# Performance work log

Hardware: AMD Instinct MI355X
Metric: run time of the kernel (lower is better)

Reference implementation:

```python
import jax, jax.numpy as jnp
import numpy as np

EPS = 1e-5

def _ln(x, g, b, axes):
    mu = x.mean(axis=axes, keepdims=True)
    var = ((x - mu) ** 2).mean(axis=axes, keepdims=True)
    return (x - mu) * jax.lax.rsqrt(var + EPS) * g + b

def _conv1d(x, w, b, groups=1):
    # x: (B, C, L), w: (O, I/groups, K), padding=1
    y = jax.lax.conv_general_dilated(x, w, (1,), [(1, 1)],
                                     dimension_numbers=('NCH', 'OIH', 'NCH'),
                                     feature_group_count=groups)
    return y + b[None, :, None]

def _gelu(x):
    return jax.nn.gelu(x, approximate=False)

def _ssm(x, xproj_w, xproj_b, A, D, sn_g, sn_b):
    # x: (B, L, d_inner)
    n = A.shape[-1]
    xp = jnp.einsum('bld,nd->bln', x, xproj_w) + xproj_b   # (B, L, 2n)
    Bp = jnp.tanh(xp[..., :n])
    Cp = jnp.tanh(xp[..., n:])
    tA = jnp.tanh(A)                                        # (d_inner, n)
    Bsz, L, di = x.shape
    state0 = jnp.zeros((Bsz, di, n), x.dtype)

    def step(state, inputs):
        Bt, Ct, xt = inputs                 # (B,n), (B,n), (B,di)
        state = state + Bt[:, None, :]      # broadcast over d_inner
        out = jnp.einsum('bdn,bn->bd', state, Ct) + xt * D
        state = state * tA[None]
        state = _ln(state, sn_g, sn_b, (1, 2))  # LayerNorm over [d_inner, d_state]
        return state, out

    xs = (jnp.swapaxes(Bp, 0, 1), jnp.swapaxes(Cp, 0, 1), jnp.swapaxes(x, 0, 1))
    _, ys = jax.lax.scan(step, state0, xs)  # ys: (L, B, di)
    return jnp.swapaxes(ys, 0, 1)

def _mamba_block(h, inproj_w, inproj_b, dw_w, dw_b, xproj_w, xproj_b, A, D, sn_g, sn_b, outproj_w, outproj_b):
    di = dw_w.shape[0]
    xp = jnp.einsum('bld,ed->ble', h, inproj_w) + inproj_b  # (B, L, 2*di)
    x_conv, x_res = xp[..., :di], xp[..., di:]
    x_conv = _gelu(_conv1d(jnp.swapaxes(x_conv, 1, 2), dw_w, dw_b, groups=di))
    x_conv = jnp.swapaxes(x_conv, 1, 2)
    y = _ssm(x_conv, xproj_w, xproj_b, A, D, sn_g, sn_b)
    y = y * _gelu(x_res)
    return jnp.einsum('bld,od->blo', y, outproj_w) + outproj_b

def setup_inputs() -> dict:
    key = jax.random.key(0)
    ks = jax.random.split(key, 10)
    B, L, Cin, dm, nl, di, n, nc = 128, 400, 8, 256, 2, 512, 16, 37
    rn = lambda k, shp, s: jax.random.normal(k, shp, jnp.float32) * s
    return {
        'x': jax.random.normal(ks[0], (B, L, Cin), jnp.float32),
        'conv1_w': rn(ks[1], (dm, Cin, 3), 0.1), 'conv1_b': jnp.zeros((dm,), jnp.float32),
        'conv2_w': rn(ks[2], (dm, dm, 3), 0.05), 'conv2_b': jnp.zeros((dm,), jnp.float32),
        'ln_g': jnp.ones((nl, dm), jnp.float32), 'ln_b': jnp.zeros((nl, dm), jnp.float32),
        'inproj_w': rn(ks[3], (nl, 2 * di, dm), 0.02), 'inproj_b': jnp.zeros((nl, 2 * di), jnp.float32),
        'dw_w': rn(ks[4], (nl, di, 1, 3), 0.1), 'dw_b': jnp.zeros((nl, di), jnp.float32),
        'xproj_w': rn(ks[5], (nl, 2 * n, di), 0.02), 'xproj_b': jnp.zeros((nl, 2 * n), jnp.float32),
        'A': jnp.full((nl, di, n), 0.1, jnp.float32), 'D': jnp.ones((nl, di), jnp.float32),
        'sn_g': jnp.ones((nl, di, n), jnp.float32), 'sn_b': jnp.zeros((nl, di, n), jnp.float32),
        'outproj_w': rn(ks[6], (nl, dm, di), 0.02), 'outproj_b': jnp.zeros((nl, dm), jnp.float32),
        'fc_w': rn(ks[7], (nc, dm), 0.02), 'fc_b': jnp.zeros((nc,), jnp.float32),
    }

def reference(x, conv1_w, conv1_b, conv2_w, conv2_b, ln_g, ln_b, inproj_w, inproj_b,
              dw_w, dw_b, xproj_w, xproj_b, A, D, sn_g, sn_b, outproj_w, outproj_b,
              fc_w, fc_b):
    h = jnp.swapaxes(x, 1, 2)                      # (B, Cin, L)
    h = jax.nn.relu(_conv1d(h, conv1_w, conv1_b))
    h = jax.nn.relu(_conv1d(h, conv2_w, conv2_b))
    h = jnp.swapaxes(h, 1, 2)                      # (B, L, d_model)
    n_layers = ln_g.shape[0]
    for i in range(n_layers):
        hn = _ln(h, ln_g[i], ln_b[i], (-1,))
        h = h + _mamba_block(hn, inproj_w[i], inproj_b[i], dw_w[i], dw_b[i],
                             xproj_w[i], xproj_b[i], A[i], D[i], sn_g[i], sn_b[i],
                             outproj_w[i], outproj_b[i])
    pooled = h.mean(axis=1)                        # (B, d_model)
    return pooled @ fc_w.T + fc_b                  # (B, num_classes)
```

## Files before the change

kernel.cpp:

```cpp
#include <hip/hip_runtime.h>
#include <hip/hip_bf16.h>
#include <math.h>

#define DEVINL __device__ __forceinline__

typedef __attribute__((ext_vector_type(2))) float  f32x2;
typedef __attribute__((ext_vector_type(4))) float  f32x4;
typedef __attribute__((ext_vector_type(8))) __bf16 bf16x8;
typedef __attribute__((ext_vector_type(8))) unsigned short ushort8;

DEVINL float b2f(unsigned short u) {
    union { unsigned int i; float f; } v; v.i = ((unsigned int)u) << 16; return v.f;
}
DEVINL unsigned short f2b(float f) {
    union { float f; unsigned int i; } v; v.f = f;
    unsigned int u = v.i;
    unsigned int r = (u + 0x7fffu + ((u >> 16) & 1u)) >> 16;
    return (unsigned short)r;
}
DEVINL float gelu_exact(float x) {
    return 0.5f * x * (1.0f + erff(x * 0.70710678118654752440f));
}

DEVINL f32x2 pk_fma(f32x2 a, f32x2 b, f32x2 c) {
    f32x2 d; asm("v_pk_fma_f32 %0, %1, %2, %3" : "=v"(d) : "v"(a), "v"(b), "v"(c)); return d;
}
DEVINL f32x2 pk_add(f32x2 a, f32x2 b) {
    f32x2 d; asm("v_pk_add_f32 %0, %1, %2" : "=v"(d) : "v"(a), "v"(b)); return d;
}
DEVINL f32x2 pk_mul(f32x2 a, f32x2 b) {
    f32x2 d; asm("v_pk_mul_f32 %0, %1, %2" : "=v"(d) : "v"(a), "v"(b)); return d;
}

DEVINL void bar_lgkm() {
    asm volatile("s_waitcnt lgkmcnt(0)" ::: "memory");
    __builtin_amdgcn_s_barrier();
    __builtin_amdgcn_sched_barrier(0);
}

DEVINL int swz(int off) { return off ^ (((off >> 6) & 7) << 3); }

DEVINL void gload16(const unsigned short* g, unsigned short* l) {
    __builtin_amdgcn_global_load_lds(
        (const __attribute__((address_space(1))) unsigned int*)g,
        (__attribute__((address_space(3))) unsigned int*)l, 16, 0, 0);
}

template <int CTRL>
DEVINL float dpp_add(float x) {
    int xi = __builtin_bit_cast(int, x);
    int yi = __builtin_amdgcn_update_dpp(0, xi, CTRL, 0xf, 0xf, true);
    return x + __builtin_bit_cast(float, yi);
}
DEVINL float wave_sum63(float x) {
    x = dpp_add<0x111>(x);
    x = dpp_add<0x112>(x);
    x = dpp_add<0x114>(x);
    x = dpp_add<0x118>(x);
    x = dpp_add<0x142>(x);
    x = dpp_add<0x143>(x);
    return x;
}

__global__ __launch_bounds__(256) void conv1_kernel(
    const float* __restrict__ x, const float* __restrict__ w,
    const float* __restrict__ bias, unsigned short* __restrict__ h1)
{
    __shared__ float xs[52 * 8];
    int b = blockIdx.x >> 3, tile = blockIdx.x & 7;
    int p0 = tile * 50;
    int t = threadIdx.x;
    for (int i = t; i < 416; i += 256) {
        int p = i >> 3, c = i & 7;
        int lp = p0 + p - 1;
        xs[i] = (lp >= 0 && lp < 400) ? x[((size_t)b * 400 + lp) * 8 + c] : 0.0f;
    }
    float wr[24];
    const float4* wp = (const float4*)(w + t * 24);
#pragma unroll
    for (int i = 0; i < 6; ++i) {
        float4 v4 = wp[i];
        wr[i * 4] = v4.x; wr[i * 4 + 1] = v4.y; wr[i * 4 + 2] = v4.z; wr[i * 4 + 3] = v4.w;
    }
    float bs = bias[t];
    __syncthreads();
#pragma unroll 2
    for (int p = 0; p < 50; ++p) {
        float acc = bs;
#pragma unroll
        for (int dt = 0; dt < 3; ++dt)
#pragma unroll
            for (int c = 0; c < 8; ++c)
                acc += xs[(p + dt) * 8 + c] * wr[c * 3 + dt];
        h1[((size_t)b * 400 + p0 + p) * 256 + t] = f2b(fmaxf(acc, 0.0f));
    }
}

__global__ void reorder_w2_kernel(const float* __restrict__ w, unsigned short* __restrict__ out)
{
    int idx = blockIdx.x * 256 + threadIdx.x;
    if (idx >= 256 * 768) return;
    int o = idx / 768, r = idx % 768;
    int tpos = r / 256, ci = r % 256;
    out[idx] = f2b(w[o * 768 + ci * 3 + tpos]);
}

__global__ void castw_kernel(const float* __restrict__ in, unsigned short* __restrict__ out, int n)
{
    int i = blockIdx.x * 256 + threadIdx.x;
    if (i < n) out[i] = f2b(in[i]);
}

__global__ __launch_bounds__(256) void ln_kernel(
    const float* __restrict__ h, const float* __restrict__ g,
    const float* __restrict__ bta, unsigned short* __restrict__ out)
{
    int w = threadIdx.x >> 6, l = threadIdx.x & 63;
    int row = blockIdx.x * 4 + w;
    const float* p = h + (size_t)row * 256 + l * 4;
    float4 v = *(const float4*)p;
    float s  = v.x + v.y + v.z + v.w;
    float s2 = v.x * v.x + v.y * v.y + v.z * v.z + v.w * v.w;
#pragma unroll
    for (int m = 1; m < 64; m <<= 1) { s += __shfl_xor(s, m); s2 += __shfl_xor(s2, m); }
    float mu = s * (1.0f / 256.0f);
    float var = s2 * (1.0f / 256.0f) - mu * mu;
    float rs = rsqrtf(var + 1e-5f);
    float4 gg = *(const float4*)(g + l * 4);
    float4 bb = *(const float4*)(bta + l * 4);
    ushort4 o;
    o.x = f2b((v.x - mu) * rs * gg.x + bb.x);
    o.y = f2b((v.y - mu) * rs * gg.y + bb.y);
    o.z = f2b((v.z - mu) * rs * gg.z + bb.z);
    o.w = f2b((v.w - mu) * rs * gg.w + bb.w);
    *(ushort4*)(out + (size_t)row * 256 + l * 4) = o;
}

template <int EPI>
__global__ __launch_bounds__(256) void gemm_bt(
    const unsigned short* __restrict__ A, const unsigned short* __restrict__ Bt,
    const float* __restrict__ bias, const float* __restrict__ res,
    void* __restrict__ Cout, int N, int K, int lda, int ldc)
{
    __shared__ unsigned short As[128 * 64];
    __shared__ unsigned short Bs[128 * 64];
    const int nbn = N >> 7;
    int bm = blockIdx.x / nbn, bn = blockIdx.x % nbn;
    int t = threadIdx.x, l = t & 63, w = t >> 6;
    int wm = w & 1, wn = w >> 1;
    int srow = t >> 3;
    int scol = 8 * ((t & 7) ^ ((t >> 3) & 7));
    f32x4 acc[4][4] = {};
    const int ktn = K >> 6;
    for (int kt = 0; kt < ktn; ++kt) {
#pragma unroll
        for (int i = 0; i < 4; ++i) {
            int row = i * 32 + srow;
            gload16(A + (size_t)(bm * 128 + row) * lda + kt * 64 + scol,
                    As + (i * 256 + w * 64) * 8);
            gload16(Bt + (size_t)(bn * 128 + row) * K + kt * 64 + scol,
                    Bs + (i * 256 + w * 64) * 8);
        }
        __syncthreads();
#pragma unroll
        for (int kk = 0; kk < 2; ++kk) {
            bf16x8 af[4], bfr[4];
#pragma unroll
            for (int i = 0; i < 4; ++i) {
                af[i]  = *(const bf16x8*)(As + swz((wm * 64 + i * 16 + (l & 15)) * 64 + kk * 32 + (l >> 4) * 8));
                bfr[i] = *(const bf16x8*)(Bs + swz((wn * 64 + i * 16 + (l & 15)) * 64 + kk * 32 + (l >> 4) * 8));
            }
#pragma unroll
            for (int i = 0; i < 4; ++i)
#pragma unroll
                for (int j = 0; j < 4; ++j)
                    acc[i][j] = __builtin_amdgcn_mfma_f32_16x16x32_bf16(af[i], bfr[j], acc[i][j], 0, 0, 0);
        }
        __syncthreads();
    }
    int r0 = bm * 128 + wm * 64 + (l >> 4) * 4;
    int c0 = bn * 128 + wn * 64 + (l & 15);
#pragma unroll
    for (int i = 0; i < 4; ++i) {
#pragma unroll
        for (int j = 0; j < 4; ++j) {
            int col = c0 + j * 16;
            float bb = bias[col];
#pragma unroll
            for (int q = 0; q < 4; ++q) {
                int row = r0 + i * 16 + q;
                float v = acc[i][j][q] + bb;
                if (EPI == 0) {
                    ((unsigned short*)Cout)[(size_t)row * ldc + col] = f2b(v);
                } else if (EPI == 1) {
                    ((unsigned short*)Cout)[(size_t)row * ldc + col] = f2b(gelu_exact(v));
                } else if (EPI == 3) {
                    size_t idx = (size_t)row * ldc + col;
                    ((float*)Cout)[idx] = v + res[idx];
                } else {
                    if (col < 512)
                        ((unsigned short*)Cout)[(size_t)row * 512 + col] = f2b(v);
                    else
                        ((unsigned short*)res)[(size_t)row * 512 + (col - 512)] = f2b(gelu_exact(v));
                }
            }
        }
    }
}

__global__ __launch_bounds__(256) void gemm_conv2(
    const unsigned short* __restrict__ h1, const unsigned short* __restrict__ Bt,
    const float* __restrict__ bias, float* __restrict__ Cout)
{
    __shared__ unsigned short As[128 * 64];
    __shared__ unsigned short Bs[128 * 64];
    int bm = blockIdx.x >> 1, bn = blockIdx.x & 1;
    int t = threadIdx.x, l = t & 63, w = t >> 6;
    int wm = w & 1, wn = w >> 1;
    f32x4 acc[4][4] = {};
    for (int kt = 0; kt < 12; ++kt) {
        int tpos = kt >> 2;
        int cbase = (kt & 3) * 64;
#pragma unroll
        for (int i = 0; i < 4; ++i) {
            int off = (i * 256 + t) * 8;
            int row = off >> 6, col = off & 63;
            int m = bm * 128 + row;
            int b = m / 400, ll = m % 400;
            int lp = ll + tpos - 1;
            ushort8 va = (ushort8)0;
            if (lp >= 0 && lp < 400)
                va = *(const ushort8*)(h1 + ((size_t)(b * 400 + lp) * 256 + cbase + col));
            *(ushort8*)(As + swz(off)) = va;
            ushort8 vb = *(const ushort8*)(Bt + (size_t)(bn * 128 + row) * 768 + kt * 64 + col);
            *(ushort8*)(Bs + swz(off)) = vb;
        }
        __syncthreads();
#pragma unroll
        for (int kk = 0; kk < 2; ++kk) {
            bf16x8 af[4], bfr[4];
#pragma unroll
            for (int i = 0; i < 4; ++i) {
                af[i]  = *(const bf16x8*)(As + swz((wm * 64 + i * 16 + (l & 15)) * 64 + kk * 32 + (l >> 4) * 8));
                bfr[i] = *(const bf16x8*)(Bs + swz((wn * 64 + i * 16 + (l & 15)) * 64 + kk * 32 + (l >> 4) * 8));
            }
#pragma unroll
            for (int i = 0; i < 4; ++i)
#pragma unroll
                for (int j = 0; j < 4; ++j)
                    acc[i][j] = __builtin_amdgcn_mfma_f32_16x16x32_bf16(af[i], bfr[j], acc[i][j], 0, 0, 0);
        }
        __syncthreads();
    }
    int r0 = bm * 128 + wm * 64 + (l >> 4) * 4;
    int c0 = bn * 128 + wn * 64 + (l & 15);
#pragma unroll
    for (int i = 0; i < 4; ++i)
#pragma unroll
        for (int j = 0; j < 4; ++j) {
            int col = c0 + j * 16;
            float bb = bias[col];
#pragma unroll
            for (int q = 0; q < 4; ++q) {
                int row = r0 + i * 16 + q;
                Cout[(size_t)row * 256 + col] = fmaxf(acc[i][j][q] + bb, 0.0f);
            }
        }
}

__global__ __launch_bounds__(256) void dwconv_kernel(
    const unsigned short* __restrict__ xp, const float* __restrict__ w,
    const float* __restrict__ bias, unsigned short* __restrict__ out)
{
    int b = blockIdx.x >> 3, tile = blockIdx.x & 7;
    int p0 = tile * 50;
    int t = threadIdx.x;
    int c = t * 2;
    float w00 = w[c * 3], w01 = w[c * 3 + 1], w02 = w[c * 3 + 2];
    float w10 = w[c * 3 + 3], w11 = w[c * 3 + 4], w12 = w[c * 3 + 5];
    float b0 = bias[c], b1 = bias[c + 1];
    const size_t rowb = (size_t)b * 400;
    int l = p0;
    unsigned int r0 = (l - 1 >= 0) ? *(const unsigned int*)(xp + (rowb + l - 1) * 512 + c) : 0u;
    unsigned int r1 = *(const unsigned int*)(xp + (rowb + l) * 512 + c);
    for (int q = 0; q < 50; ++q, ++l) {
        unsigned int r2 = (l + 1 < 400) ? *(const unsigned int*)(xp + (rowb + l + 1) * 512 + c) : 0u;
        float a0 = b0 + b2f((unsigned short)(r0 & 0xffff)) * w00
                      + b2f((unsigned short)(r1 & 0xffff)) * w01
                      + b2f((unsigned short)(r2 & 0xffff)) * w02;
        float a1 = b1 + b2f((unsigned short)(r0 >> 16)) * w10
                      + b2f((unsigned short)(r1 >> 16)) * w11
                      + b2f((unsigned short)(r2 >> 16)) * w12;
        unsigned int o = (unsigned int)f2b(gelu_exact(a0)) | ((unsigned int)f2b(gelu_exact(a1)) << 16);
        *(unsigned int*)(out + (rowb + l) * 512 + c) = o;
        r0 = r1; r1 = r2;
    }
}

__global__ __launch_bounds__(256) void xproj_mfma(
    const unsigned short* __restrict__ xc, const unsigned short* __restrict__ w,
    const float* __restrict__ bias, float* __restrict__ BC)
{
    __shared__ unsigned short As[128 * 64];
    __shared__ unsigned short Bs[32 * 64];
    int bm = blockIdx.x;
    int t = threadIdx.x, l = t & 63, wv = t >> 6;
    f32x4 acc[2][2] = {};
    for (int kt = 0; kt < 8; ++kt) {
#pragma unroll
        for (int i = 0; i < 4; ++i) {
            int off = (i * 256 + t) * 8;
            int row = off >> 6, col = off & 63;
            ushort8 va = *(const ushort8*)(xc + (size_t)(bm * 128 + row) * 512 + kt * 64 + col);
            *(ushort8*)(As + swz(off)) = va;
        }
        {
            int off = t * 8;
            int row = off >> 6, col = off & 63;
            ushort8 vb = *(const ushort8*)(w + (size_t)row * 512 + kt * 64 + col);
            *(ushort8*)(Bs + swz(off)) = vb;
        }
        __syncthreads();
#pragma unroll
        for (int kk = 0; kk < 2; ++kk) {
            bf16x8 af[2], bfr[2];
#pragma unroll
            for (int i = 0; i < 2; ++i) {
                af[i]  = *(const bf16x8*)(As + swz((wv * 32 + i * 16 + (l & 15)) * 64 + kk * 32 + (l >> 4) * 8));
                bfr[i] = *(const bf16x8*)(Bs + swz((i * 16 + (l & 15)) * 64 + kk * 32 + (l >> 4) * 8));
            }
#pragma unroll
            for (int i = 0; i < 2; ++i)
#pragma unroll
                for (int j = 0; j < 2; ++j)
                    acc[i][j] = __builtin_amdgcn_mfma_f32_16x16x32_bf16(af[i], bfr[j], acc[i][j], 0, 0, 0);
        }
        __syncthreads();
    }
    int r0 = bm * 128 + wv * 32 + (l >> 4) * 4;
    int c0 = l & 15;
#pragma unroll
    for (int i = 0; i < 2; ++i)
#pragma unroll
        for (int j = 0; j < 2; ++j) {
            int col = c0 + j * 16;
            float bb = bias[col];
#pragma unroll
            for (int q = 0; q < 4; ++q) {
                int row = r0 + i * 16 + q;
                BC[(size_t)row * 32 + col] = tanhf(acc[i][j][q] + bb);
            }
        }
}

__global__ __launch_bounds__(512) void scan_kernel(
    const float* __restrict__ BC, const unsigned short* __restrict__ xconv,
    const unsigned short* __restrict__ gres, const float* __restrict__ Aw,
    const float* __restrict__ Dw, const float* __restrict__ sng,
    const float* __restrict__ snb, unsigned short* __restrict__ yg)
{
    __shared__ __align__(16) unsigned short lds_x[2][4096];
    __shared__ __align__(16) unsigned short lds_g[2][4096];
    __shared__ __align__(16) float lds_bc[2][256];
    __shared__ __align__(16) float lds_s1[2][8];
    __shared__ __align__(16) float lds_s2[2][8];
    int b = blockIdx.x, t = threadIdx.x;
    f32x2 st2[8], tA2[8], g2[8], bb2[8];
#pragma unroll
    for (int j = 0; j < 8; ++j) {
        st2[j] = (f32x2)(0.0f);
        f32x2 av = *(const f32x2*)(Aw + t * 16 + j * 2);
        tA2[j] = (f32x2){tanhf(av.x), tanhf(av.y)};
        g2[j]  = *(const f32x2*)(sng + t * 16 + j * 2);
        bb2[j] = *(const f32x2*)(snb + t * 16 + j * 2);
    }
    float Dd = Dw[t];
    const size_t base = (size_t)b * 400;
    {
        size_t o = base * 512 + t * 8;
        *(ushort8*)(&lds_x[0][t * 8]) = *(const ushort8*)(xconv + o);
        *(ushort8*)(&lds_g[0][t * 8]) = *(const ushort8*)(gres + o);
        if (t < 64) *(float4*)(&lds_bc[0][t * 4]) = *(const float4*)(BC + base * 32 + t * 4);
    }
    bar_lgkm();
    int cur = 0;
    ushort8 xs_r, gs_r; float4 bc_r;
    for (int l = 0; l < 400; ++l) {
        int p = l & 7;
        if (p == 0 && l + 8 < 400) {
            size_t o = (base + l + 8) * 512 + t * 8;
            xs_r = *(const ushort8*)(xconv + o);
            gs_r = *(const ushort8*)(gres + o);
            if (t < 64) bc_r = *(const float4*)(BC + (base + l + 8) * 32 + t * 4);
        }
        const f32x2* bcp = (const f32x2*)(&lds_bc[cur][p * 32]);
        f32x2 B2[8], C2[8];
#pragma unroll
        for (int q = 0; q < 8; ++q) { B2[q] = bcp[q]; C2[q] = bcp[8 + q]; }
        float xt = b2f(lds_x[cur][p * 512 + t]);
        float gr = b2f(lds_g[cur][p * 512 + t]);
        f32x2 oA = (f32x2){xt * Dd, 0.0f}, oB = (f32x2)(0.0f);
#pragma unroll
        for (int j = 0; j < 8; j += 2) {
            st2[j]     = pk_add(st2[j],     B2[j]);     oA = pk_fma(st2[j],     C2[j],     oA);
            st2[j + 1] = pk_add(st2[j + 1], B2[j + 1]); oB = pk_fma(st2[j + 1], C2[j + 1], oB);
        }
        f32x2 oS = pk_add(oA, oB);
        yg[(base + l) * 512 + t] = f2b((oS.x + oS.y) * gr);
        f32x2 sA = (f32x2)(0.0f), sB = (f32x2)(0.0f), qA = (f32x2)(0.0f), qB = (f32x2)(0.0f);
#pragma unroll
        for (int j = 0; j < 8; j += 2) {
            st2[j]     = pk_mul(st2[j],     tA2[j]);
            st2[j + 1] = pk_mul(st2[j + 1], tA2[j + 1]);
            sA = pk_add(sA, st2[j]);     qA = pk_fma(st2[j],     st2[j],     qA);
            sB = pk_add(sB, st2[j + 1]); qB = pk_fma(st2[j + 1], st2[j + 1], qB);
        }
        f32x2 sS = pk_add(sA, sB), qS = pk_add(qA, qB);
        float s1 = wave_sum63(sS.x + sS.y);
        float s2 = wave_sum63(qS.x + qS.y);
        if (p == 7 && l + 1 < 400) {
            *(ushort8*)(&lds_x[cur ^ 1][t * 8]) = xs_r;
            *(ushort8*)(&lds_g[cur ^ 1][t * 8]) = gs_r;
            if (t < 64) *(float4*)(&lds_bc[cur ^ 1][t * 4]) = bc_r;
        }
        if ((t & 63) == 63) { lds_s1[l & 1][t >> 6] = s1; lds_s2[l & 1][t >> 6] = s2; }
        bar_lgkm();
        float4 p0v = *(const float4*)&lds_s1[l & 1][0];
        float4 p1v = *(const float4*)&lds_s1[l & 1][4];
        float4 r0v = *(const float4*)&lds_s2[l & 1][0];
        float4 r1v = *(const float4*)&lds_s2[l & 1][4];
        float S1 = ((p0v.x + p0v.y) + (p0v.z + p0v.w)) + ((p1v.x + p1v.y) + (p1v.z + p1v.w));
        float S2 = ((r0v.x + r0v.y) + (r0v.z + r0v.w)) + ((r1v.x + r1v.y) + (r1v.z + r1v.w));
        float mu = S1 * (1.0f / 8192.0f);
        float var = S2 * (1.0f / 8192.0f) - mu * mu;
        float rs = rsqrtf(var + 1e-5f);
        f32x2 rs2 = (f32x2){rs, rs};
        f32x2 nm2 = (f32x2){-mu * rs, -mu * rs};
#pragma unroll
        for (int j = 0; j < 8; ++j) {
            f32x2 zn = pk_fma(st2[j], rs2, nm2);
            st2[j] = pk_fma(zn, g2[j], bb2[j]);
        }
        if (p == 7) cur ^= 1;
    }
}

__global__ __launch_bounds__(256) void poolfc_kernel(
    const float* __restrict__ h, const float* __restrict__ fcw,
    const float* __restrict__ fcb, float* __restrict__ out)
{
    __shared__ float ps[256];
    int b = blockIdx.x, t = threadIdx.x;
    float s = 0.0f;
    for (int l = 0; l < 400; ++l) s += h[((size_t)b * 400 + l) * 256 + t];
    ps[t] = s * (1.0f / 400.0f);
    __syncthreads();
    if (t < 37) {
        float acc = fcb[t];
        for (int o = 0; o < 256; ++o) acc += ps[o] * fcw[t * 256 + o];
        out[b * 37 + t] = acc;
    }
}

extern "C" void kernel_launch(void* const* d_in, const int* in_sizes, int n_in,
                              void* d_out, int out_size, void* d_ws, size_t ws_size,
                              hipStream_t stream)
{
    const float* x         = (const float*)d_in[0];
    const float* conv1_w   = (const float*)d_in[1];
    const float* conv1_b   = (const float*)d_in[2];
    const float* conv2_w   = (const float*)d_in[3];
    const float* conv2_b   = (const float*)d_in[4];
    const float* ln_g      = (const float*)d_in[5];
    const float* ln_b      = (const float*)d_in[6];
    const float* inproj_w  = (const float*)d_in[7];
    const float* inproj_b  = (const float*)d_in[8];
    const float* dw_w      = (const float*)d_in[9];
    const float* dw_b      = (const float*)d_in[10];
    const float* xproj_w   = (const float*)d_in[11];
    const float* xproj_b   = (const float*)d_in[12];
    const float* A         = (const float*)d_in[13];
    const float* D         = (const float*)d_in[14];
    const float* sn_g      = (const float*)d_in[15];
    const float* sn_b      = (const float*)d_in[16];
    const float* outproj_w = (const float*)d_in[17];
    const float* outproj_b = (const float*)d_in[18];
    const float* fc_w      = (const float*)d_in[19];
    const float* fc_b      = (const float*)d_in[20];
    float* out = (float*)d_out;

    const int M = 51200;

    if (ws_size < 243007488u) return;
    char* ws = (char*)d_ws;
    float*          h    = (float*)(ws);
    unsigned short* hn   = (unsigned short*)(ws + 52428800);
    unsigned short* h1   = (unsigned short*)(ws + 52428800);
    unsigned short* xp_c = (unsigned short*)(ws + 78643200);
    unsigned short* yg   = (unsigned short*)(ws + 78643200);
    unsigned short* grs  = (unsigned short*)(ws + 131072000);
    unsigned short* xcv  = (unsigned short*)(ws + 183500800);
    float*          BC   = (float*)(ws + 235929600);
    unsigned short* wbuf = (unsigned short*)(ws + 242483200);

    conv1_kernel<<<128 * 8, 256, 0, stream>>>(x, conv1_w, conv1_b, h1);
    reorder_w2_kernel<<<768, 256, 0, stream>>>(conv2_w, wbuf);
    gemm_conv2<<<(M / 128) * 2, 256, 0, stream>>>(h1, wbuf, conv2_b, h);

    for (int i = 0; i < 2; ++i) {
        ln_kernel<<<M / 4, 256, 0, stream>>>(h, ln_g + i * 256, ln_b + i * 256, hn);
        castw_kernel<<<1024, 256, 0, stream>>>(inproj_w + (size_t)i * 262144, wbuf, 262144);
        gemm_bt<4><<<(M / 128) * 8, 256, 0, stream>>>(hn, wbuf, inproj_b + i * 1024,
                                                      (const float*)grs, xp_c, 1024, 256, 256, 512);
        dwconv_kernel<<<1024, 256, 0, stream>>>(xp_c, dw_w + i * 1536, dw_b + i * 512, xcv);
        castw_kernel<<<64, 256, 0, stream>>>(xproj_w + i * 16384, wbuf, 16384);
        xproj_mfma<<<M / 128, 256, 0, stream>>>(xcv, wbuf, xproj_b + i * 32, BC);
        scan_kernel<<<128, 512, 0, stream>>>(BC, xcv, grs, A + i * 8192, D + i * 512,
                                             sn_g + i * 8192, sn_b + i * 8192, yg);
        castw_kernel<<<512, 256, 0, stream>>>(outproj_w + (size_t)i * 131072, wbuf, 131072);
        gemm_bt<3><<<(M / 128) * 2, 256, 0, stream>>>(yg, wbuf, outproj_b + i * 256, h, h,
                                                      256, 512, 512, 256);
    }
    poolfc_kernel<<<128, 256, 0, stream>>>(h, fc_w, fc_b, out);
}
```

Measured before the change: 1.002 ms.

## Software-pipeline SSM scan LDS reads across the per-step barrier

Result: no change. 982.6 us (-1.9%).

```diff
diff --git a/kernel.cpp b/kernel.cpp
--- a/kernel.cpp
+++ b/kernel.cpp
@@ -383,65 +383,100 @@
         if (t < 64) *(float4*)(&lds_bc[0][t * 4]) = *(const float4*)(BC + base * 32 + t * 4);
     }
     bar_lgkm();
-    int cur = 0;
+    float4 bcv[8];
+#pragma unroll
+    for (int q = 0; q < 8; ++q) bcv[q] = *(const float4*)&lds_bc[0][q * 4];
+    unsigned short cxr = lds_x[0][t], cgr = lds_g[0][t];
     ushort8 xs_r, gs_r; float4 bc_r;
-    for (int l = 0; l < 400; ++l) {
-        int p = l & 7;
-        if (p == 0 && l + 8 < 400) {
-            size_t o = (base + l + 8) * 512 + t * 8;
-            xs_r = *(const ushort8*)(xconv + o);
-            gs_r = *(const ushort8*)(gres + o);
-            if (t < 64) bc_r = *(const float4*)(BC + (base + l + 8) * 32 + t * 4);
-        }
-        const f32x2* bcp = (const f32x2*)(&lds_bc[cur][p * 32]);
-        f32x2 B2[8], C2[8];
-#pragma unroll
-        for (int q = 0; q < 8; ++q) { B2[q] = bcp[q]; C2[q] = bcp[8 + q]; }
-        float xt = b2f(lds_x[cur][p * 512 + t]);
-        float gr = b2f(lds_g[cur][p * 512 + t]);
-        f32x2 oA = (f32x2){xt * Dd, 0.0f}, oB = (f32x2)(0.0f);
-#pragma unroll
-        for (int j = 0; j < 8; j += 2) {
-            st2[j]     = pk_add(st2[j],     B2[j]);     oA = pk_fma(st2[j],     C2[j],     oA);
-            st2[j + 1] = pk_add(st2[j + 1], B2[j + 1]); oB = pk_fma(st2[j + 1], C2[j + 1], oB);
-        }
-        f32x2 oS = pk_add(oA, oB);
-        yg[(base + l) * 512 + t] = f2b((oS.x + oS.y) * gr);
-        f32x2 sA = (f32x2)(0.0f), sB = (f32x2)(0.0f), qA = (f32x2)(0.0f), qB = (f32x2)(0.0f);
-#pragma unroll
-        for (int j = 0; j < 8; j += 2) {
-            st2[j]     = pk_mul(st2[j],     tA2[j]);
-            st2[j + 1] = pk_mul(st2[j + 1], tA2[j + 1]);
-            sA = pk_add(sA, st2[j]);     qA = pk_fma(st2[j],     st2[j],     qA);
-            sB = pk_add(sB, st2[j + 1]); qB = pk_fma(st2[j + 1], st2[j + 1], qB);
-        }
-        f32x2 sS = pk_add(sA, sB), qS = pk_add(qA, qB);
-        float s1 = wave_sum63(sS.x + sS.y);
-        float s2 = wave_sum63(qS.x + qS.y);
-        if (p == 7 && l + 1 < 400) {
-            *(ushort8*)(&lds_x[cur ^ 1][t * 8]) = xs_r;
-            *(ushort8*)(&lds_g[cur ^ 1][t * 8]) = gs_r;
-            if (t < 64) *(float4*)(&lds_bc[cur ^ 1][t * 4]) = bc_r;
-        }
-        if ((t & 63) == 63) { lds_s1[l & 1][t >> 6] = s1; lds_s2[l & 1][t >> 6] = s2; }
-        bar_lgkm();
-        float4 p0v = *(const float4*)&lds_s1[l & 1][0];
-        float4 p1v = *(const float4*)&lds_s1[l & 1][4];
-        float4 r0v = *(const float4*)&lds_s2[l & 1][0];
-        float4 r1v = *(const float4*)&lds_s2[l & 1][4];
-        float S1 = ((p0v.x + p0v.y) + (p0v.z + p0v.w)) + ((p1v.x + p1v.y) + (p1v.z + p1v.w));
-        float S2 = ((r0v.x + r0v.y) + (r0v.z + r0v.w)) + ((r1v.x + r1v.y) + (r1v.z + r1v.w));
-        float mu = S1 * (1.0f / 8192.0f);
-        float var = S2 * (1.0f / 8192.0f) - mu * mu;
-        float rs = rsqrtf(var + 1e-5f);
-        f32x2 rs2 = (f32x2){rs, rs};
-        f32x2 nm2 = (f32x2){-mu * rs, -mu * rs};
-#pragma unroll
-        for (int j = 0; j < 8; ++j) {
-            f32x2 zn = pk_fma(st2[j], rs2, nm2);
-            st2[j] = pk_fma(zn, g2[j], bb2[j]);
-        }
-        if (p == 7) cur ^= 1;
+    for (int c = 0; c < 50; ++c) {
+        int cur = c & 1;
+        const size_t lbase = base + c * 8;
+#pragma unroll
+        for (int pp = 0; pp < 8; ++pp) {
+            if (pp == 0 && c + 1 < 50) {
+                size_t o = (lbase + 8) * 512 + t * 8;
+                xs_r = *(const ushort8*)(xconv + o);
+                gs_r = *(const ushort8*)(gres + o);
+                if (t < 64) bc_r = *(const float4*)(BC + (lbase + 8) * 32 + t * 4);
+            }
+            const f32x2* Bp = (const f32x2*)&bcv[0];
+            const f32x2* Cp = (const f32x2*)&bcv[4];
+            float cx = b2f(cxr), cg = b2f(cgr);
+            f32x2 oA = (f32x2){cx * Dd, 0.0f}, oB = (f32x2)(0.0f);
+#pragma unroll
+            for (int j = 0; j < 8; j += 2) {
+                st2[j]     = pk_add(st2[j],     Bp[j]);     oA = pk_fma(st2[j],     Cp[j],     oA);
+                st2[j + 1] = pk_add(st2[j + 1], Bp[j + 1]); oB = pk_fma(st2[j + 1], Cp[j + 1], oB);
+            }
+            f32x2 oS = pk_add(oA, oB);
+            yg[(lbase + pp) * 512 + t] = f2b((oS.x + oS.y) * cg);
+            f32x2 sA = (f32x2)(0.0f), sB = (f32x2)(0.0f), qA = (f32x2)(0.0f), qB = (f32x2)(0.0f);
+#pragma unroll
+            for (int j = 0; j < 8; j += 2) {
+                st2[j]     = pk_mul(st2[j],     tA2[j]);
+                st2[j + 1] = pk_mul(st2[j + 1], tA2[j + 1]);
+                sA = pk_add(sA, st2[j]);     qA = pk_fma(st2[j],     st2[j],     qA);
+                sB = pk_add(sB, st2[j + 1]); qB = pk_fma(st2[j + 1], st2[j + 1], qB);
+            }
+            f32x2 sS = pk_add(sA, sB), qS = pk_add(qA, qB);
+            float s1 = wave_sum63(sS.x + sS.y);
+            float s2 = wave_sum63(qS.x + qS.y);
+            if (pp == 6 && c + 1 < 50) {
+                if (t < 64) *(float4*)(&lds_bc[cur ^ 1][t * 4]) = bc_r;
+            }
+            if (pp == 7 && c + 1 < 50) {
+                *(ushort8*)(&lds_x[cur ^ 1][t * 8]) = xs_r;
+                *(ushort8*)(&lds_g[cur ^ 1][t * 8]) = gs_r;
+            }
+            if ((t & 63) == 63) { lds_s1[pp & 1][t >> 6] = s1; lds_s2[pp & 1][t >> 6] = s2; }
+            __builtin_amdgcn_sched_barrier(0);
+            float4 nbc[8]; unsigned short nxr = 0, ngr = 0;
+            if (pp < 7) {
+#pragma unroll
+                for (int q = 0; q < 8; ++q)
+                    nbc[q] = *(const float4*)&lds_bc[cur][(pp + 1) * 32 + q * 4];
+                nxr = lds_x[cur][(pp + 1) * 512 + t];
+                ngr = lds_g[cur][(pp + 1) * 512 + t];
+                __builtin_amdgcn_sched_barrier(0);
+                asm volatile("s_waitcnt lgkmcnt(10)" ::: "memory");
+            } else if (c + 1 < 50) {
+#pragma unroll
+                for (int q = 0; q < 8; ++q)
+                    nbc[q] = *(const float4*)&lds_bc[cur ^ 1][q * 4];
+                __builtin_amdgcn_sched_barrier(0);
+                asm volatile("s_waitcnt lgkmcnt(8)" ::: "memory");
+            } else {
+                asm volatile("s_waitcnt lgkmcnt(0)" ::: "memory");
+            }
+            __builtin_amdgcn_s_barrier();
+            __builtin_amdgcn_sched_barrier(0);
+            float4 p0v = *(const float4*)&lds_s1[pp & 1][0];
+            float4 p1v = *(const float4*)&lds_s1[pp & 1][4];
+            float4 r0v = *(const float4*)&lds_s2[pp & 1][0];
+            float4 r1v = *(const float4*)&lds_s2[pp & 1][4];
+            float S1 = ((p0v.x + p0v.y) + (p0v.z + p0v.w)) + ((p1v.x + p1v.y) + (p1v.z + p1v.w));
+            float S2 = ((r0v.x + r0v.y) + (r0v.z + r0v.w)) + ((r1v.x + r1v.y) + (r1v.z + r1v.w));
+            float mu = S1 * (1.0f / 8192.0f);
+            float var = S2 * (1.0f / 8192.0f) - mu * mu;
+            float rs = rsqrtf(var + 1e-5f);
+            f32x2 rs2 = (f32x2){rs, rs};
+            f32x2 nm2 = (f32x2){-mu * rs, -mu * rs};
+#pragma unroll
+            for (int j = 0; j < 8; ++j) {
+                f32x2 zn = pk_fma(st2[j], rs2, nm2);
+                st2[j] = pk_fma(zn, g2[j], bb2[j]);
+            }
+            if (pp < 7) {
+#pragma unroll
+                for (int q = 0; q < 8; ++q) bcv[q] = nbc[q];
+                cxr = nxr; cgr = ngr;
+            } else if (c + 1 < 50) {
+#pragma unroll
+                for (int q = 0; q < 8; ++q) bcv[q] = nbc[q];
+                cxr = lds_x[cur ^ 1][t];
+                cgr = lds_g[cur ^ 1][t];
+            }
+        }
     }
 }
 
```
